# Kernel optimization log

Measured on AMD Instinct MI355X. Metric: run time of the kernel, lower is better.

Reference implementation:

```python
import jax, jax.numpy as jnp
import numpy as np

NUM_HEADS = 16


def setup_inputs() -> dict:
    key = jax.random.key(0)
    ks = jax.random.split(key, 4)
    B, C, T, D = 1, 1, 3072, 1024
    s = 1.0 / np.sqrt(D)
    return {
        "x": jax.random.normal(ks[0], (B, C, T, D), dtype=jnp.float32),
        "Wq": jax.random.normal(ks[1], (D, D), dtype=jnp.float32) * s,
        "bq": jnp.zeros((D,), dtype=jnp.float32),
        "Wk": jax.random.normal(ks[2], (D, D), dtype=jnp.float32) * s,
        "bk": jnp.zeros((D,), dtype=jnp.float32),
        "Wv": jax.random.normal(ks[3], (D, D), dtype=jnp.float32) * s,
        "bv": jnp.zeros((D,), dtype=jnp.float32),
        "gamma": jnp.float32(0.5),  # learned scalar; 0.0 at torch init, nonzero here for a meaningful signal
    }


def reference(x, Wq, bq, Wk, bk, Wv, bv, gamma):
    # x: (B, C, T, D); Linear acts on last dim (torch: y = x @ W.T + b)
    B, C, T, D = x.shape
    H = NUM_HEADS
    q = (jnp.einsum("bctd,ed->bcte", x, Wq) + bq).reshape(B, -1, T, H)  # (B, X, T, H), X = C*D/H
    k = (jnp.einsum("bctd,ed->bcte", x, Wk) + bk).reshape(B, -1, T, H)
    v = (jnp.einsum("bctd,ed->bcte", x, Wv) + bv).reshape(B, -1, T, H)
    q = q.transpose(0, 3, 2, 1)  # (B, H, T, X)
    k = k.transpose(0, 3, 1, 2)  # (B, H, X, T)
    energy = q @ k               # (B, H, T, T)  -- note: NO 1/sqrt(d) scaling, as in source
    attn = jax.nn.softmax(energy, axis=-1)
    v = v.transpose(0, 3, 2, 1)  # (B, H, T, X)
    out = attn @ v               # (B, H, T, X)
    out = out.transpose(0, 2, 3, 1).reshape(B, T, -1)  # (B, T, X*H) = (B, T, C*D)
    # residual broadcast: (B, T, C*D) + (B, C, T, D); valid since B == C == 1
    return gamma * out + x
```

## Files before the change

### kernel.cpp

```cpp
#include <hip/hip_runtime.h>


typedef _Float16 v8h __attribute__((ext_vector_type(8)));
typedef _Float16 v4h __attribute__((ext_vector_type(4)));
typedef __fp16   v2pk __attribute__((ext_vector_type(2)));
typedef __fp16   v4pk __attribute__((ext_vector_type(4)));
typedef float    v4f __attribute__((ext_vector_type(4)));

#define TSEQ 3072
#define DM   1024
#define NH   16
#define XD   64
#define LOG2E 1.44269504f

__device__ __forceinline__ void async_load16(const void* g, void* l) {
  __builtin_amdgcn_global_load_lds(
      (const __attribute__((address_space(1))) unsigned int*)g,
      (__attribute__((address_space(3))) unsigned int*)l,
      16, 0, 0);
}

__device__ __forceinline__ float fexp2(float x) {
  float r; asm("v_exp_f32 %0, %1" : "=v"(r) : "v"(x)); return r;
}
__device__ __forceinline__ float flog2(float x) {
  float r; asm("v_log_f32 %0, %1" : "=v"(r) : "v"(x)); return r;
}

extern "C" __global__ __launch_bounds__(256) void cvt_kernel(
    const float* __restrict__ x, const float* __restrict__ wq,
    const float* __restrict__ wk, const float* __restrict__ wv,
    _Float16* __restrict__ xb, _Float16* __restrict__ wb)
{
  const int NX4 = (TSEQ * DM) / 4;
  const int NT  = NX4 * 2;
  for (int i = blockIdx.x * blockDim.x + threadIdx.x; i < NT;
       i += gridDim.x * blockDim.x) {
    float4 v;
    _Float16* dst;
    if (i < NX4) {
      v = ((const float4*)x)[i];
      dst = xb + (size_t)i * 4;
    } else {
      const int j = i - NX4;
      const int n = j >> 8;
      if (n < 1024)      v = ((const float4*)wq)[j];
      else if (n < 2048) v = ((const float4*)wk)[j - 262144];
      else               v = ((const float4*)wv)[j - 524288];
      dst = wb + (size_t)j * 4;
    }
    v4h h;
    h[0] = (_Float16)v.x; h[1] = (_Float16)v.y;
    h[2] = (_Float16)v.z; h[3] = (_Float16)v.w;
    *(v4h*)dst = h;
  }
}

extern "C" __global__ __launch_bounds__(256) void qkv_gemm_kernel(
    const _Float16* __restrict__ xb, const _Float16* __restrict__ wb,
    const float* __restrict__ bq, const float* __restrict__ bk,
    const float* __restrict__ bv,
    _Float16* __restrict__ qlin, _Float16* __restrict__ klin,
    _Float16* __restrict__ vlin)
{
  __shared__ _Float16 As[128 * 32];
  __shared__ _Float16 Bs[128 * 32];
  const int tid = threadIdx.x;
  const int w = tid >> 6, l = tid & 63;
  const int li = l & 15, lg = l >> 4;
  const int wm = w >> 1, wn = w & 1;
  const int bid = blockIdx.x;
  const int swz = (bid & 7) * 72 + (bid >> 3);
  const int m0 = (swz / 24) * 128, n0 = (swz % 24) * 128;
  v4f acc[4][4] = {};
  const int srow = l >> 2;
  const int scol = (l & 3) * 8;
  for (int k0 = 0; k0 < DM; k0 += 32) {
#pragma unroll
    for (int c = 0; c < 2; ++c) {
      const int rbase = c * 64 + w * 16;
      async_load16(xb + (size_t)(m0 + rbase + srow) * DM + k0 + scol, &As[rbase * 32]);
      async_load16(wb + (size_t)(n0 + rbase + srow) * DM + k0 + scol, &Bs[rbase * 32]);
    }
    __syncthreads();
    v8h af[4], bf[4];
#pragma unroll
    for (int mi = 0; mi < 4; ++mi)
      af[mi] = *(const v8h*)&As[(wm * 64 + mi * 16 + li) * 32 + lg * 8];
#pragma unroll
    for (int ni = 0; ni < 4; ++ni)
      bf[ni] = *(const v8h*)&Bs[(wn * 64 + ni * 16 + li) * 32 + lg * 8];
#pragma unroll
    for (int mi = 0; mi < 4; ++mi)
#pragma unroll
      for (int ni = 0; ni < 4; ++ni)
        acc[mi][ni] = __builtin_amdgcn_mfma_f32_16x16x32_f16(
            af[mi], bf[ni], acc[mi][ni], 0, 0, 0);
    __syncthreads();
  }
  const int which = n0 >> 10;
  const int ebase = n0 & 1023;
  const float* bias = which == 0 ? bq : (which == 1 ? bk : bv);
  _Float16* outp = which == 0 ? qlin : (which == 1 ? klin : vlin);
#pragma unroll
  for (int mi = 0; mi < 4; ++mi)
#pragma unroll
    for (int r = 0; r < 4; ++r) {
      const int t = m0 + wm * 64 + mi * 16 + lg * 4 + r;
#pragma unroll
      for (int ni = 0; ni < 4; ++ni) {
        const int e = ebase + wn * 64 + ni * 16 + li;
        outp[(size_t)t * DM + e] = (_Float16)(acc[mi][ni][r] + bias[e]);
      }
    }
}

extern "C" __global__ __launch_bounds__(256) void repack_kernel(
    const _Float16* __restrict__ qlin, const _Float16* __restrict__ klin,
    const _Float16* __restrict__ vlin,
    _Float16* __restrict__ qh, _Float16* __restrict__ kh,
    _Float16* __restrict__ vt)
{
  const int NE = NH * TSEQ * XD;
  for (int g = blockIdx.x * blockDim.x + threadIdx.x; g < 3 * NE;
       g += gridDim.x * blockDim.x) {
    if (g < 2 * NE) {
      const int gg = (g < NE) ? g : g - NE;
      const int xx = gg & 63;
      const int rest = gg >> 6;
      const int h = rest / TSEQ;
      const int i = rest - h * TSEQ;
      const int t = xx * 48 + (i >> 6);
      const int e = ((i & 63) << 4) + h;
      if (g < NE) qh[gg] = qlin[t * DM + e];
      else        kh[gg] = (_Float16)((float)klin[t * DM + e] * LOG2E);
    } else {
      const int o = g - 2 * NE;
      const int j = o % TSEQ;
      const int rest = o / TSEQ;
      const int xx = rest & 63;
      const int h = rest >> 6;
      const int t = xx * 48 + (j >> 6);
      const int e = ((j & 63) << 4) + h;
      vt[o] = vlin[t * DM + e];
    }
  }
}

extern "C" __global__ __launch_bounds__(256, 2) void attn_kernel(
    const _Float16* __restrict__ qh, const _Float16* __restrict__ kh,
    const _Float16* __restrict__ vt,
    _Float16* __restrict__ oP0, _Float16* __restrict__ oP1,
    float* __restrict__ sml0, float* __restrict__ sml1)
{
  __shared__ _Float16 SH[16384];
  const int tid = threadIdx.x;
  const int w = tid >> 6, l = tid & 63;
  const int li = l & 15, lg = l >> 4;
  const int b = blockIdx.x;
  const int rest = b >> 3;
  const int head = (b & 7) + 8 * (rest & 1);
  const int qt = (rest >> 1) & 15;
  const int jh = rest >> 5;
  const int i0 = qt * 192;
  const size_t hb = (size_t)head * TSEQ * XD;
  _Float16* oPart = jh ? oP1 : oP0;
  float* smlp = jh ? sml1 : sml0;

  v8h qf[3][2];
#pragma unroll
  for (int ct = 0; ct < 3; ++ct) {
    const _Float16* qrow = qh + hb + (size_t)(i0 + w * 48 + ct * 16 + li) * XD;
    qf[ct][0] = *(const v8h*)(qrow + lg * 8);
    qf[ct][1] = *(const v8h*)(qrow + 32 + lg * 8);
  }
  float m2[3] = {24.0f * LOG2E, 24.0f * LOG2E, 24.0f * LOG2E};
  float l4[3] = {0.0f, 0.0f, 0.0f};
  v4f oacc[4][3] = {};
  const int r8 = l >> 3, c8 = l & 7;
  const int jbase = jh * 1536;

  for (int j0 = jbase; j0 < jbase + 1536; j0 += 128) {
#pragma unroll
    for (int s2 = 0; s2 < 2; ++s2) {
      const int jt = j0 + s2 * 64;
#pragma unroll
      for (int s = 0; s < 2; ++s) {
        const int n = w * 2 + s;
        const int row = n * 8 + r8;
        async_load16(kh + hb + (size_t)(jt + row) * XD + ((c8 ^ (row & 7)) * 8),
                     &SH[s2 * 4096 + n * 512]);
        async_load16(vt + hb + (size_t)row * TSEQ + jt + ((c8 ^ (row & 7)) * 8),
                     &SH[8192 + s2 * 4096 + n * 512]);
      }
    }
    __syncthreads();

#pragma unroll
    for (int s2 = 0; s2 < 2; ++s2) {
      const _Float16* Kc = &SH[s2 * 4096];
      const _Float16* Vc = &SH[8192 + s2 * 4096];

      v4f e4[3][4];
#pragma unroll
      for (int kt = 0; kt < 4; ++kt) {
        const int krow = kt * 16 + li;
        const v8h kf0 = *(const v8h*)&Kc[krow * 64 + ((lg ^ (li & 7)) * 8)];
        const v8h kf1 = *(const v8h*)&Kc[krow * 64 + (((4 + lg) ^ (li & 7)) * 8)];
#pragma unroll
        for (int ct = 0; ct < 3; ++ct) {
          v4f a = {-m2[ct], -m2[ct], -m2[ct], -m2[ct]};
          a = __builtin_amdgcn_mfma_f32_16x16x32_f16(kf0, qf[ct][0], a, 0, 0, 0);
          a = __builtin_amdgcn_mfma_f32_16x16x32_f16(kf1, qf[ct][1], a, 0, 0, 0);
          e4[ct][kt] = a;
        }
      }

      float gm = -1.0e30f;
#pragma unroll
      for (int ct = 0; ct < 3; ++ct)
#pragma unroll
        for (int kt = 0; kt < 4; ++kt)
          gm = fmaxf(fmaxf(gm, fmaxf(e4[ct][kt][0], e4[ct][kt][1])),
                     fmaxf(e4[ct][kt][2], e4[ct][kt][3]));
      if (__any(gm > 11.5f)) {
#pragma unroll
        for (int ct = 0; ct < 3; ++ct) {
          float rm = -1.0e30f;
#pragma unroll
          for (int kt = 0; kt < 4; ++kt)
            rm = fmaxf(fmaxf(rm, fmaxf(e4[ct][kt][0], e4[ct][kt][1])),
                       fmaxf(e4[ct][kt][2], e4[ct][kt][3]));
          rm = fmaxf(rm, __shfl_xor(rm, 16, 64));
          rm = fmaxf(rm, __shfl_xor(rm, 32, 64));
          rm = fmaxf(rm, 0.0f);
          const float fs = fexp2(-rm);
#pragma unroll
          for (int kt = 0; kt < 4; ++kt)
#pragma unroll
            for (int rr = 0; rr < 4; ++rr) e4[ct][kt][rr] -= rm;
          l4[ct] *= fs;
#pragma unroll
          for (int mi = 0; mi < 4; ++mi) oacc[mi][ct] *= fs;
          m2[ct] += rm;
        }
      }

      v4h pv[3][4];
#pragma unroll
      for (int ct = 0; ct < 3; ++ct) {
#pragma unroll
        for (int kt = 0; kt < 4; ++kt) {
          const float p0 = fexp2(e4[ct][kt][0]);
          const float p1 = fexp2(e4[ct][kt][1]);
          const float p2 = fexp2(e4[ct][kt][2]);
          const float p3 = fexp2(e4[ct][kt][3]);
          const v2pk lo = __builtin_amdgcn_cvt_pkrtz(p0, p1);
          const v2pk hi = __builtin_amdgcn_cvt_pkrtz(p2, p3);
          const v4pk pk = __builtin_shufflevector(lo, hi, 0, 1, 2, 3);
          pv[ct][kt] = __builtin_bit_cast(v4h, pk);
          l4[ct] += (p0 + p1) + (p2 + p3);
        }
      }

#pragma unroll
      for (int mi = 0; mi < 4; ++mi) {
        const int vrow = mi * 16 + li;
        const int vb = vrow * 64 + (lg & 1) * 4;
#pragma unroll
        for (int kt = 0; kt < 4; ++kt) {
          const v4h vf = *(const v4h*)&Vc[vb + (((kt * 2 + (lg >> 1)) ^ (li & 7)) * 8)];
#pragma unroll
          for (int ct = 0; ct < 3; ++ct)
            oacc[mi][ct] = __builtin_amdgcn_mfma_f32_16x16x16f16(
                vf, pv[ct][kt], oacc[mi][ct], 0, 0, 0);
        }
      }
    }
    __syncthreads();
  }

#pragma unroll
  for (int ct = 0; ct < 3; ++ct) {
    float ls = l4[ct];
    ls += __shfl_xor(ls, 16, 64);
    ls += __shfl_xor(ls, 32, 64);
    const float inv = 1.0f / ls;
    const int rl = w * 48 + ct * 16 + li;
    if (lg == 0) smlp[(size_t)(i0 + rl) * NH + head] = m2[ct] + flog2(ls);
#pragma unroll
    for (int mi = 0; mi < 4; ++mi) {
      v4h o4;
#pragma unroll
      for (int rr = 0; rr < 4; ++rr) o4[rr] = (_Float16)(oacc[mi][ct][rr] * inv);
      *(v4h*)&oPart[(size_t)(i0 + rl) * DM + head * 64 + mi * 16 + lg * 4] = o4;
    }
  }
}

extern "C" __global__ __launch_bounds__(256) void epilogue_kernel(
    const _Float16* __restrict__ oP0, const _Float16* __restrict__ oP1,
    const float* __restrict__ sml0, const float* __restrict__ sml1,
    const float* __restrict__ xin, const float* __restrict__ gscal,
    float* __restrict__ outp)
{
  __shared__ float po[8 * 1024];
  const int tid = threadIdx.x;
  const size_t t0 = (size_t)blockIdx.x * 8;
  {
    const int tr = tid >> 5;
    const int c0 = (tid & 31) * 32;
    const int h = c0 >> 6;
    const size_t t = t0 + tr;
    const float s0 = sml0[t * NH + h], s1 = sml1[t * NH + h];
    const float M = fmaxf(s0, s1);
    float u0 = fexp2(s0 - M), u1 = fexp2(s1 - M);
    const float dn = 1.0f / (u0 + u1);
    u0 *= dn; u1 *= dn;
    const _Float16* p0 = oP0 + t * DM + c0;
    const _Float16* p1 = oP1 + t * DM + c0;
#pragma unroll
    for (int c = 0; c < 4; ++c) {
      const v8h a = *(const v8h*)(p0 + c * 8);
      const v8h bb = *(const v8h*)(p1 + c * 8);
      float acc[8];
#pragma unroll
      for (int e = 0; e < 8; ++e)
        acc[e] = u0 * (float)a[e] + u1 * (float)bb[e];
      float4 w0 = {acc[0], acc[1], acc[2], acc[3]};
      float4 w1 = {acc[4], acc[5], acc[6], acc[7]};
      *(float4*)&po[tr * 1024 + c0 + c * 8]     = w0;
      *(float4*)&po[tr * 1024 + c0 + c * 8 + 4] = w1;
    }
  }
  __syncthreads();
  const float g = gscal[0];
  const int tr = tid >> 5;
  const int d0 = (tid & 31) * 32;
  const size_t rb = (t0 + tr) * DM + d0;
#pragma unroll
  for (int c4 = 0; c4 < 8; ++c4) {
    const float4 xi = *(const float4*)&xin[rb + c4 * 4];
    float4 rr;
    rr.x = g * po[tr * 1024 + ((c4 * 4 + 0) & 15) * 64 + ((d0 + c4 * 4 + 0) >> 4)] + xi.x;
    rr.y = g * po[tr * 1024 + ((c4 * 4 + 1) & 15) * 64 + ((d0 + c4 * 4 + 1) >> 4)] + xi.y;
    rr.z = g * po[tr * 1024 + ((c4 * 4 + 2) & 15) * 64 + ((d0 + c4 * 4 + 2) >> 4)] + xi.z;
    rr.w = g * po[tr * 1024 + ((c4 * 4 + 3) & 15) * 64 + ((d0 + c4 * 4 + 3) >> 4)] + xi.w;
    *(float4*)&outp[rb + c4 * 4] = rr;
  }
}

extern "C" void kernel_launch(void* const* d_in, const int* in_sizes, int n_in,
                              void* d_out, int out_size, void* d_ws, size_t ws_size,
                              hipStream_t stream)
{
  const float* x  = (const float*)d_in[0];
  const float* Wq = (const float*)d_in[1];
  const float* bq = (const float*)d_in[2];
  const float* Wk = (const float*)d_in[3];
  const float* bk = (const float*)d_in[4];
  const float* Wv = (const float*)d_in[5];
  const float* bv = (const float*)d_in[6];
  const float* gm = (const float*)d_in[7];
  float* outp = (float*)d_out;
  char* ws = (char*)d_ws;
  const size_t SZH = (size_t)TSEQ * DM * sizeof(_Float16);
  _Float16* xb   = (_Float16*)(ws);
  _Float16* wb   = (_Float16*)(ws + SZH);
  _Float16* qlin = (_Float16*)(ws + 2 * SZH);
  _Float16* klin = (_Float16*)(ws + 3 * SZH);
  _Float16* vlin = (_Float16*)(ws + 4 * SZH);
  _Float16* qhp  = (_Float16*)(ws + 5 * SZH);
  _Float16* khp  = (_Float16*)(ws + 6 * SZH);
  _Float16* vtp  = (_Float16*)(ws + 7 * SZH);
  _Float16* oP0  = (_Float16*)(ws);
  _Float16* oP1  = (_Float16*)(ws + SZH);
  float*    sml0 = (float*)(ws + 3 * SZH);
  float*    sml1 = sml0 + (size_t)TSEQ * NH;

  cvt_kernel<<<dim3(1024), dim3(256), 0, stream>>>(x, Wq, Wk, Wv, xb, wb);
  qkv_gemm_kernel<<<dim3(576), dim3(256), 0, stream>>>(xb, wb, bq, bk, bv,
                                                       qlin, klin, vlin);
  repack_kernel<<<dim3(4096), dim3(256), 0, stream>>>(qlin, klin, vlin,
                                                      qhp, khp, vtp);
  attn_kernel<<<dim3(512), dim3(256), 0, stream>>>(qhp, khp, vtp,
                                                   oP0, oP1, sml0, sml1);
  epilogue_kernel<<<dim3(384), dim3(256), 0, stream>>>(oP0, oP1, sml0, sml1,
                                                       x, gm, outp);
  (void)in_sizes; (void)n_in; (void)out_size; (void)ws_size;
}
```

Measured before the change: 133.2 us.

## Deepen QKV GEMM K-tile with swizzled LDS; compute softmax row sums via MFMA

The QKV projection GEMM now stages 64-wide K slices per iteration instead of 32, using an XOR-swizzled shared-memory layout to avoid bank conflicts. This halves the number of barrier pairs per tile. In the attention kernel, the per-lane scalar accumulation of softmax denominators is replaced by an MFMA against a ones vector, removing VALU adds and the final cross-lane shuffles. The cost is extra MFMA issue slots and doubled LDS use in the GEMM, which may lower occupancy.

```diff
diff --git a/kernel.cpp b/kernel.cpp
--- a/kernel.cpp
+++ b/kernel.cpp
@@ -63,8 +63,8 @@
     _Float16* __restrict__ qlin, _Float16* __restrict__ klin,
     _Float16* __restrict__ vlin)
 {
-  __shared__ _Float16 As[128 * 32];
-  __shared__ _Float16 Bs[128 * 32];
+  __shared__ _Float16 As[128 * 64];
+  __shared__ _Float16 Bs[128 * 64];
   const int tid = threadIdx.x;
   const int w = tid >> 6, l = tid & 63;
   const int li = l & 15, lg = l >> 4;
@@ -73,29 +73,37 @@
   const int swz = (bid & 7) * 72 + (bid >> 3);
   const int m0 = (swz / 24) * 128, n0 = (swz % 24) * 128;
   v4f acc[4][4] = {};
-  const int srow = l >> 2;
-  const int scol = (l & 3) * 8;
-  for (int k0 = 0; k0 < DM; k0 += 32) {
-#pragma unroll
-    for (int c = 0; c < 2; ++c) {
-      const int rbase = c * 64 + w * 16;
-      async_load16(xb + (size_t)(m0 + rbase + srow) * DM + k0 + scol, &As[rbase * 32]);
-      async_load16(wb + (size_t)(n0 + rbase + srow) * DM + k0 + scol, &Bs[rbase * 32]);
+  const int r8 = l >> 3, c8 = l & 7;
+  for (int k0 = 0; k0 < DM; k0 += 64) {
+#pragma unroll
+    for (int c = 0; c < 4; ++c) {
+      const int n = w * 4 + c;
+      const int row = n * 8 + r8;
+      const int ss = (c8 ^ r8) * 8;
+      async_load16(xb + (size_t)(m0 + row) * DM + k0 + ss, &As[n * 512]);
+      async_load16(wb + (size_t)(n0 + row) * DM + k0 + ss, &Bs[n * 512]);
     }
     __syncthreads();
-    v8h af[4], bf[4];
-#pragma unroll
-    for (int mi = 0; mi < 4; ++mi)
-      af[mi] = *(const v8h*)&As[(wm * 64 + mi * 16 + li) * 32 + lg * 8];
-#pragma unroll
-    for (int ni = 0; ni < 4; ++ni)
-      bf[ni] = *(const v8h*)&Bs[(wn * 64 + ni * 16 + li) * 32 + lg * 8];
-#pragma unroll
-    for (int mi = 0; mi < 4; ++mi)
-#pragma unroll
-      for (int ni = 0; ni < 4; ++ni)
-        acc[mi][ni] = __builtin_amdgcn_mfma_f32_16x16x32_f16(
-            af[mi], bf[ni], acc[mi][ni], 0, 0, 0);
+#pragma unroll
+    for (int kk = 0; kk < 2; ++kk) {
+      v8h af[4], bf[4];
+#pragma unroll
+      for (int mi = 0; mi < 4; ++mi) {
+        const int row = wm * 64 + mi * 16 + li;
+        af[mi] = *(const v8h*)&As[row * 64 + (((kk * 4 + lg) ^ (li & 7)) * 8)];
+      }
+#pragma unroll
+      for (int ni = 0; ni < 4; ++ni) {
+        const int row = wn * 64 + ni * 16 + li;
+        bf[ni] = *(const v8h*)&Bs[row * 64 + (((kk * 4 + lg) ^ (li & 7)) * 8)];
+      }
+#pragma unroll
+      for (int mi = 0; mi < 4; ++mi)
+#pragma unroll
+        for (int ni = 0; ni < 4; ++ni)
+          acc[mi][ni] = __builtin_amdgcn_mfma_f32_16x16x32_f16(
+              af[mi], bf[ni], acc[mi][ni], 0, 0, 0);
+    }
     __syncthreads();
   }
   const int which = n0 >> 10;
@@ -174,8 +182,9 @@
     qf[ct][0] = *(const v8h*)(qrow + lg * 8);
     qf[ct][1] = *(const v8h*)(qrow + 32 + lg * 8);
   }
+  const v4h ones = {(_Float16)1.0f, (_Float16)1.0f, (_Float16)1.0f, (_Float16)1.0f};
   float m2[3] = {24.0f * LOG2E, 24.0f * LOG2E, 24.0f * LOG2E};
-  float l4[3] = {0.0f, 0.0f, 0.0f};
+  v4f l4a[3] = {};
   v4f oacc[4][3] = {};
   const int r8 = l >> 3, c8 = l & 7;
   const int jbase = jh * 1536;
@@ -239,7 +248,7 @@
           for (int kt = 0; kt < 4; ++kt)
 #pragma unroll
             for (int rr = 0; rr < 4; ++rr) e4[ct][kt][rr] -= rm;
-          l4[ct] *= fs;
+          l4a[ct] *= fs;
 #pragma unroll
           for (int mi = 0; mi < 4; ++mi) oacc[mi][ct] *= fs;
           m2[ct] += rm;
@@ -259,9 +268,15 @@
           const v2pk hi = __builtin_amdgcn_cvt_pkrtz(p2, p3);
           const v4pk pk = __builtin_shufflevector(lo, hi, 0, 1, 2, 3);
           pv[ct][kt] = __builtin_bit_cast(v4h, pk);
-          l4[ct] += (p0 + p1) + (p2 + p3);
         }
       }
+
+#pragma unroll
+      for (int ct = 0; ct < 3; ++ct)
+#pragma unroll
+        for (int kt = 0; kt < 4; ++kt)
+          l4a[ct] = __builtin_amdgcn_mfma_f32_16x16x16f16(
+              ones, pv[ct][kt], l4a[ct], 0, 0, 0);
 
 #pragma unroll
       for (int mi = 0; mi < 4; ++mi) {
@@ -282,9 +297,7 @@
 
 #pragma unroll
   for (int ct = 0; ct < 3; ++ct) {
-    float ls = l4[ct];
-    ls += __shfl_xor(ls, 16, 64);
-    ls += __shfl_xor(ls, 32, 64);
+    const float ls = l4a[ct][0];
     const float inv = 1.0f / ls;
     const int rl = w * 48 + ct * 16 + li;
     if (lg == 0) smlp[(size_t)(i0 + rl) * NH + head] = m2[ct] + flog2(ls);
```

Measured after the change: 147.0 us. 1.1x slower.
